# Optimization experiments

Measured on AMD Instinct MI355X. Metric: run time of the kernel, lower is better.

The kernel has to match this reference:

```python
import jax, jax.numpy as jnp
import numpy as np

N_HEADS = 8
EPSILON = -50000.0


def setup_inputs() -> dict:
    key = jax.random.key(0)
    k1, k2, k3, k4, k5, k6 = jax.random.split(key, 6)
    B, S, D = 4, 2048, 512
    q_vec = jax.random.normal(k1, (B, S, D), dtype=jnp.float32)
    k_mat = jax.random.normal(k2, (B, S, D), dtype=jnp.float32)
    v_mat = jax.random.normal(k3, (B, S, D), dtype=jnp.float32)
    # mask: mostly valid keys with some padding masked out
    mask = jax.random.uniform(k4, (B, S)) < 0.9
    cutoff = jax.random.uniform(k5, (B, S), dtype=jnp.float32)
    W_out = jax.random.normal(k6, (D, D), dtype=jnp.float32) * (1.0 / np.sqrt(D))
    return {"q_vec": q_vec, "k_mat": k_mat, "v_mat": v_mat,
            "mask": mask, "cutoff": cutoff, "W_out": W_out}


def reference(q_vec, k_mat, v_mat, mask, cutoff, W_out):
    D = q_vec.shape[-1]
    H = N_HEADS
    dh = D // H
    # split heads: [B, S, D] -> [B, S, H, dh]
    q_ = q_vec.reshape(q_vec.shape[:-1] + (H, dh))
    k_ = k_mat.reshape(k_mat.shape[:-1] + (H, dh))
    v_ = v_mat.reshape(v_mat.shape[:-1] + (H, dh))
    # scores: [B, H, Sq, Sk]
    scores = jnp.einsum('bqhd,bkhd->bhqk', q_, k_) / jnp.sqrt(jnp.asarray(dh, q_vec.dtype))
    # additive mask over keys, then stable softmax
    scores = jnp.where(mask[:, None, None, :], scores, EPSILON)
    probs = jax.nn.softmax(scores, axis=-1)
    # post-softmax cutoff scaling per key
    probs = probs * cutoff[:, None, None, :]
    # attention output: [B, Sq, H, dh] -> [B, Sq, D]
    att = jnp.einsum('bhqk,bkhd->bqhd', probs, v_).reshape(q_vec.shape)
    return att @ W_out
```

## Files before the change

kernel.cpp:

```cpp
#include <hip/hip_runtime.h>
#include <hip/hip_bf16.h>
#include <stdint.h>

#define B_ 4
#define S_ 2048
#define D_ 512
#define H_ 8

typedef __attribute__((ext_vector_type(4))) float f32x4;
typedef __attribute__((ext_vector_type(16))) float f32x16;
typedef __attribute__((ext_vector_type(8))) short s16x8;

__device__ __forceinline__ unsigned short f2bf(float x) {
  union { float f; unsigned u; } v; v.f = x;
  unsigned r = v.u + 0x7FFFu + ((v.u >> 16) & 1u);
  return (unsigned short)(r >> 16);
}

__device__ __forceinline__ unsigned cvtpk_bf16(float lo, float hi) {
  unsigned r;
  asm("v_cvt_pk_bf16_f32 %0, %1, %2" : "=v"(r) : "v"(lo), "v"(hi));
  return r;
}

__device__ __forceinline__ void plswap(unsigned &a, unsigned &b) {
  asm("v_permlane32_swap_b32 %0, %1" : "+v"(a), "+v"(b));
}

__device__ __forceinline__ void gload16(const void* g, void* lds) {
  __builtin_amdgcn_global_load_lds(
      (const __attribute__((address_space(1))) void*)g,
      (__attribute__((address_space(3))) void*)lds, 16, 0, 0);
}

__global__ __launch_bounds__(256) void conv_kv_kernel(
    const float* __restrict__ km, const float* __restrict__ vm,
    const float* __restrict__ cut, const int* __restrict__ mask,
    unsigned short* __restrict__ Kbf, unsigned short* __restrict__ Vt,
    unsigned short* __restrict__ fmg)
{
  const int st = blockIdx.x, bh = blockIdx.y;
  const int b = bh >> 3, h = bh & 7;
  const int s0 = st * 64;
  __shared__ unsigned short sT[64][68];
  const int tid = threadIdx.x;
#pragma unroll
  for (int j = 0; j < 4; ++j) {
    const int li = tid + j * 256;
    const int r  = li >> 4;
    const int c4 = (li & 15) * 4;
    const size_t g = ((size_t)(b * S_ + s0 + r)) * D_ + h * 64 + c4;
    const float4 kv = *(const float4*)(km + g);
    const float4 vv = *(const float4*)(vm + g);
    const int mk = mask[(size_t)b * S_ + s0 + r];
    const float f = mk ? cut[(size_t)b * S_ + s0 + r] : 0.f;
    *(ushort4*)(Kbf + ((size_t)(bh * S_ + s0 + r)) * 64 + c4) =
        make_ushort4(f2bf(kv.x), f2bf(kv.y), f2bf(kv.z), f2bf(kv.w));
    sT[r][c4 + 0] = f2bf(vv.x * f);
    sT[r][c4 + 1] = f2bf(vv.y * f);
    sT[r][c4 + 2] = f2bf(vv.z * f);
    sT[r][c4 + 3] = f2bf(vv.w * f);
    if (h == 0 && c4 == 0)
      fmg[(size_t)b * S_ + s0 + r] = mk ? (unsigned short)0x3F80 : (unsigned short)0;
  }
  __syncthreads();
#pragma unroll
  for (int j = 0; j < 4; ++j) {
    const int li = tid + j * 256;
    const int dh = li >> 4;
    const int s4 = (li & 15) * 4;
    *(ushort4*)(Vt + ((size_t)(bh * 64 + dh)) * S_ + s0 + s4) =
        make_ushort4(sT[s4 + 0][dh], sT[s4 + 1][dh], sT[s4 + 2][dh], sT[s4 + 3][dh]);
  }
}

__global__ __launch_bounds__(256) void conv_w_kernel(
    const float* __restrict__ W, unsigned short* __restrict__ Wt)
{
  const int k0 = blockIdx.x * 64, n0 = blockIdx.y * 64;
  __shared__ unsigned short sT[64][68];
  const int tid = threadIdx.x;
#pragma unroll
  for (int j = 0; j < 4; ++j) {
    const int li = tid + j * 256;
    const int r  = li >> 4;
    const int c4 = (li & 15) * 4;
    const float4 wv = *(const float4*)(W + (size_t)(k0 + r) * 512 + n0 + c4);
    sT[r][c4 + 0] = f2bf(wv.x);
    sT[r][c4 + 1] = f2bf(wv.y);
    sT[r][c4 + 2] = f2bf(wv.z);
    sT[r][c4 + 3] = f2bf(wv.w);
  }
  __syncthreads();
#pragma unroll
  for (int j = 0; j < 4; ++j) {
    const int li = tid + j * 256;
    const int n  = li >> 4;
    const int k4 = (li & 15) * 4;
    *(ushort4*)(Wt + (size_t)(n0 + n) * 512 + k0 + k4) =
        make_ushort4(sT[k4 + 0][n], sT[k4 + 1][n], sT[k4 + 2][n], sT[k4 + 3][n]);
  }
}

__global__ __launch_bounds__(256, 2) void attn_mfma_kernel(
    const float* __restrict__ qv, const unsigned short* __restrict__ Kbf,
    const unsigned short* __restrict__ Vt, const unsigned short* __restrict__ fmg,
    unsigned short* __restrict__ attb)
{
  __shared__ unsigned short sK[2][2][4096];
  __shared__ unsigned short sV[2][2][4096];

  const int qt = blockIdx.x, bh = blockIdx.y;
  const int b = bh >> 3, h = bh & 7;
  const int tid = threadIdx.x, w = tid >> 6, l = tid & 63;
  const int l31 = l & 31, hi = l >> 5;
  const int qh = w & 1, kh = w >> 1;
  const int kbase = kh * 1024;

  s16x8 qf[2][4];
#pragma unroll
  for (int s = 0; s < 2; ++s) {
    const int qrow = qt * 128 + qh * 64 + s * 32 + l31;
    const float* qp = qv + ((size_t)(b * S_ + qrow)) * D_ + h * 64 + hi * 8;
#pragma unroll
    for (int kc = 0; kc < 4; ++kc) {
      const float4 a0 = *(const float4*)(qp + kc * 16);
      const float4 a1 = *(const float4*)(qp + kc * 16 + 4);
      union { unsigned u[4]; s16x8 v; } t;
      t.u[0] = cvtpk_bf16(a0.x * 0.125f, a0.y * 0.125f);
      t.u[1] = cvtpk_bf16(a0.z * 0.125f, a0.w * 0.125f);
      t.u[2] = cvtpk_bf16(a1.x * 0.125f, a1.y * 0.125f);
      t.u[3] = cvtpk_bf16(a1.z * 0.125f, a1.w * 0.125f);
      qf[s][kc] = t.v;
    }
  }

  f32x16 o00, o01, o10, o11, la0, la1;
#pragma unroll
  for (int r = 0; r < 16; ++r) {
    o00[r] = 0.f; o01[r] = 0.f; o10[r] = 0.f; o11[r] = 0.f;
    la0[r] = 0.f; la1[r] = 0.f;
  }

  const int swl = ((l & 7) ^ (l >> 3)) * 16;
  const int r8  = l >> 3;
  const char* KbfB = (const char*)(Kbf + (size_t)bh * S_ * 64);
  const char* VtB  = (const char*)(Vt + (size_t)bh * 64 * S_);

  auto STAGE = [&](int bufi, int kt) {
    const int k0 = kbase + kt * 64;
#pragma unroll
    for (int c = 0; c < 4; ++c) {
      const int chunk = qh * 4 + c;
      const int row = chunk * 8 + r8;
      gload16(KbfB + (size_t)(k0 + row) * 128 + swl, (char*)sK[kh][bufi] + chunk * 1024);
      gload16(VtB + ((size_t)row * S_ + k0) * 2 + swl, (char*)sV[kh][bufi] + chunk * 1024);
    }
  };

  STAGE(0, 0);
  __syncthreads();

  int buf = 0;
  for (int kt = 0; kt < 16; ++kt) {
    const int k0 = kbase + kt * 64;
    s16x8 fmf[4];
#pragma unroll
    for (int ks = 0; ks < 4; ++ks)
      fmf[ks] = *(const s16x8*)(fmg + (size_t)b * S_ + k0 + ks * 16 + hi * 8);

    if (kt + 1 < 16) STAGE(buf ^ 1, kt + 1);

    const char* pK = (const char*)sK[kh][buf];
    const char* pV = (const char*)sV[kh][buf];

    s16x8 pa[2][4];
#pragma unroll
    for (int k2 = 0; k2 < 2; ++k2) {
      f32x16 sa0, sa1;
#pragma unroll
      for (int r = 0; r < 16; ++r) { sa0[r] = 0.f; sa1[r] = 0.f; }
      __builtin_amdgcn_s_setprio(1);
#pragma unroll
      for (int kc = 0; kc < 4; ++kc) {
        const int row = k2 * 32 + l31;
        const s16x8 kf = *(const s16x8*)(pK + row * 128 +
                          ((kc * 32 + hi * 16) ^ ((row & 7) << 4)));
        sa0 = __builtin_amdgcn_mfma_f32_32x32x16_bf16(kf, qf[0][kc], sa0, 0, 0, 0);
        sa1 = __builtin_amdgcn_mfma_f32_32x32x16_bf16(kf, qf[1][kc], sa1, 0, 0, 0);
      }
      __builtin_amdgcn_s_setprio(0);
      float p0[16], p1[16];
#pragma unroll
      for (int r = 0; r < 16; ++r) { p0[r] = __expf(sa0[r]); p1[r] = __expf(sa1[r]); }
#pragma unroll
      for (int ks = 0; ks < 2; ++ks) {
        const int rb = ks * 8;
        {
          unsigned a0 = cvtpk_bf16(p0[rb + 0], p0[rb + 1]);
          unsigned a1 = cvtpk_bf16(p0[rb + 2], p0[rb + 3]);
          unsigned b0 = cvtpk_bf16(p0[rb + 4], p0[rb + 5]);
          unsigned b1 = cvtpk_bf16(p0[rb + 6], p0[rb + 7]);
          plswap(a0, b0); plswap(a1, b1);
          union { unsigned u[4]; s16x8 v; } t;
          t.u[0] = a0; t.u[1] = a1; t.u[2] = b0; t.u[3] = b1;
          pa[0][k2 * 2 + ks] = t.v;
        }
        {
          unsigned a0 = cvtpk_bf16(p1[rb + 0], p1[rb + 1]);
          unsigned a1 = cvtpk_bf16(p1[rb + 2], p1[rb + 3]);
          unsigned b0 = cvtpk_bf16(p1[rb + 4], p1[rb + 5]);
          unsigned b1 = cvtpk_bf16(p1[rb + 6], p1[rb + 7]);
          plswap(a0, b0); plswap(a1, b1);
          union { unsigned u[4]; s16x8 v; } t;
          t.u[0] = a0; t.u[1] = a1; t.u[2] = b0; t.u[3] = b1;
          pa[1][k2 * 2 + ks] = t.v;
        }
      }
    }

    __builtin_amdgcn_s_setprio(1);
#pragma unroll
    for (int ks2 = 0; ks2 < 4; ++ks2) {
      const int cb = ks2 * 32 + hi * 16;
      const int rv0 = l31, rv1 = 32 + l31;
      const s16x8 vb0 = *(const s16x8*)(pV + rv0 * 128 + (cb ^ ((rv0 & 7) << 4)));
      const s16x8 vb1 = *(const s16x8*)(pV + rv1 * 128 + (cb ^ ((rv1 & 7) << 4)));
      o00 = __builtin_amdgcn_mfma_f32_32x32x16_bf16(pa[0][ks2], vb0, o00, 0, 0, 0);
      o01 = __builtin_amdgcn_mfma_f32_32x32x16_bf16(pa[0][ks2], vb1, o01, 0, 0, 0);
      o10 = __builtin_amdgcn_mfma_f32_32x32x16_bf16(pa[1][ks2], vb0, o10, 0, 0, 0);
      o11 = __builtin_amdgcn_mfma_f32_32x32x16_bf16(pa[1][ks2], vb1, o11, 0, 0, 0);
      la0 = __builtin_amdgcn_mfma_f32_32x32x16_bf16(pa[0][ks2], fmf[ks2], la0, 0, 0, 0);
      la1 = __builtin_amdgcn_mfma_f32_32x32x16_bf16(pa[1][ks2], fmf[ks2], la1, 0, 0, 0);
    }
    __builtin_amdgcn_s_setprio(0);

    __syncthreads();
    buf ^= 1;
  }

  float* po = (float*)&sK[0][0][0];
  float* pl = (float*)&sV[0][0][0];

  if (kh == 0) {
#pragma unroll
    for (int half = 0; half < 2; ++half)
#pragma unroll
      for (int r = 0; r < 16; ++r) {
        po[(((qh * 2 + 0) * 2 + half) * 16 + r) * 64 + l] = (half == 0) ? o00[r] : o01[r];
        po[(((qh * 2 + 1) * 2 + half) * 16 + r) * 64 + l] = (half == 0) ? o10[r] : o11[r];
      }
    if (l31 == 0) {
#pragma unroll
      for (int r = 0; r < 16; ++r) {
        pl[((qh * 2 + 0) * 2 + hi) * 16 + r] = la0[r];
        pl[((qh * 2 + 1) * 2 + hi) * 16 + r] = la1[r];
      }
    }
  }
  __syncthreads();
  if (kh == 1) {
#pragma unroll
    for (int half = 0; half < 2; ++half)
#pragma unroll
      for (int r = 0; r < 16; ++r) {
        po[(((qh * 2 + 0) * 2 + half) * 16 + r) * 64 + l] += (half == 0) ? o00[r] : o01[r];
        po[(((qh * 2 + 1) * 2 + half) * 16 + r) * 64 + l] += (half == 0) ? o10[r] : o11[r];
      }
    if (l31 == 0) {
#pragma unroll
      for (int r = 0; r < 16; ++r) {
        pl[((qh * 2 + 0) * 2 + hi) * 16 + r] += la0[r];
        pl[((qh * 2 + 1) * 2 + hi) * 16 + r] += la1[r];
      }
    }
  }
  __syncthreads();

  const int qm = w & 1, sm = w >> 1;
  unsigned short* ob = attb + ((size_t)b * S_) * D_ + h * 64;
#pragma unroll
  for (int r = 0; r < 16; ++r) {
    const float ls = pl[((qm * 2 + sm) * 2 + hi) * 16 + r];
    const float inv = 1.f / ls;
    const int q = qt * 128 + qm * 64 + sm * 32 + (r & 3) + 8 * (r >> 2) + 4 * hi;
#pragma unroll
    for (int half = 0; half < 2; ++half) {
      const float ov = po[(((qm * 2 + sm) * 2 + half) * 16 + r) * 64 + l];
      ob[(size_t)q * D_ + half * 32 + l31] = f2bf(ov * inv);
    }
  }
}

__global__ __launch_bounds__(256) void proj_mfma_kernel(
    const unsigned short* __restrict__ A, const unsigned short* __restrict__ Wt,
    float* __restrict__ out)
{
  __shared__ unsigned short sA[128 * 64];
  __shared__ unsigned short sB[128 * 64];
  const int m0 = blockIdx.x * 128, n0 = blockIdx.y * 128;
  const int tid = threadIdx.x, w = tid >> 6, l = tid & 63;
  const int l15 = l & 15, l4 = l >> 4;
  const int wm = (w >> 1) * 64, wn = (w & 1) * 64;
  const int swl = ((l & 7) ^ (l >> 3)) * 16;
  const int r8 = l >> 3;

  f32x4 acc[4][4];
#pragma unroll
  for (int i = 0; i < 4; ++i)
#pragma unroll
    for (int j = 0; j < 4; ++j) acc[i][j] = (f32x4){0.f, 0.f, 0.f, 0.f};

  for (int kt = 0; kt < 8; ++kt) {
    const int k0 = kt * 64;
    __syncthreads();
#pragma unroll
    for (int c = 0; c < 4; ++c) {
      const int chunk = w * 4 + c;
      const int r = chunk * 8 + r8;
      gload16((const char*)(A + ((size_t)(m0 + r)) * 512 + k0) + swl,
              (char*)sA + chunk * 1024);
      gload16((const char*)(Wt + ((size_t)(n0 + r)) * 512 + k0) + swl,
              (char*)sB + chunk * 1024);
    }
    __syncthreads();
#pragma unroll
    for (int ks = 0; ks < 2; ++ks) {
      s16x8 af[4], bf_[4];
#pragma unroll
      for (int mb = 0; mb < 4; ++mb) {
        const int row = wm + mb * 16 + l15;
        const int sz = (row & 7) << 4;
        af[mb] = *(const s16x8*)((const char*)sA + row * 128 + ((ks * 64 + l4 * 16) ^ sz));
      }
#pragma unroll
      for (int nb = 0; nb < 4; ++nb) {
        const int row = wn + nb * 16 + l15;
        const int sz = (row & 7) << 4;
        bf_[nb] = *(const s16x8*)((const char*)sB + row * 128 + ((ks * 64 + l4 * 16) ^ sz));
      }
#pragma unroll
      for (int mb = 0; mb < 4; ++mb)
#pragma unroll
        for (int nb = 0; nb < 4; ++nb)
          acc[mb][nb] = __builtin_amdgcn_mfma_f32_16x16x32_bf16(af[mb], bf_[nb], acc[mb][nb], 0, 0, 0);
    }
  }
#pragma unroll
  for (int mb = 0; mb < 4; ++mb)
#pragma unroll
    for (int nb = 0; nb < 4; ++nb)
#pragma unroll
      for (int r = 0; r < 4; ++r)
        out[(size_t)(m0 + wm + mb * 16 + l4 * 4 + r) * 512 + n0 + wn + nb * 16 + l15] =
            acc[mb][nb][r];
}

extern "C" void kernel_launch(void* const* d_in, const int* in_sizes, int n_in,
                              void* d_out, int out_size, void* d_ws, size_t ws_size,
                              hipStream_t stream) {
  const float* q    = (const float*)d_in[0];
  const float* k    = (const float*)d_in[1];
  const float* v    = (const float*)d_in[2];
  const int*   mask = (const int*)d_in[3];
  const float* cut  = (const float*)d_in[4];
  const float* W    = (const float*)d_in[5];
  float* out = (float*)d_out;

  char* ws = (char*)d_ws;
  unsigned short* Kbf  = (unsigned short*)(ws);
  unsigned short* Vt   = (unsigned short*)(ws + (8u << 20));
  unsigned short* attb = (unsigned short*)(ws + (16u << 20));
  unsigned short* Wt   = (unsigned short*)(ws + (24u << 20));
  unsigned short* fmg  = (unsigned short*)(ws + (25u << 20));

  conv_kv_kernel<<<dim3(S_ / 64, B_ * H_), 256, 0, stream>>>(k, v, cut, mask, Kbf, Vt, fmg);
  conv_w_kernel<<<dim3(8, 8), 256, 0, stream>>>(W, Wt);
  attn_mfma_kernel<<<dim3(S_ / 128, B_ * H_), 256, 0, stream>>>(q, Kbf, Vt, fmg, attb);
  proj_mfma_kernel<<<dim3(64, 4), 256, 0, stream>>>(attb, Wt, out);
}
```

Before: 79.62 us.

## Halve attention query tile, use exp2 and scalar row-sum instead of MFMA sum

After: 104.6 us. 1.31x slower.

```diff
diff --git a/kernel.cpp b/kernel.cpp
--- a/kernel.cpp
+++ b/kernel.cpp
@@ -27,6 +27,12 @@
   asm("v_permlane32_swap_b32 %0, %1" : "+v"(a), "+v"(b));
 }
 
+__device__ __forceinline__ float fexp2(float x) {
+  float r;
+  asm("v_exp_f32 %0, %1" : "=v"(r) : "v"(x));
+  return r;
+}
+
 __device__ __forceinline__ void gload16(const void* g, void* lds) {
   __builtin_amdgcn_global_load_lds(
       (const __attribute__((address_space(1))) void*)g,
@@ -37,7 +43,7 @@
     const float* __restrict__ km, const float* __restrict__ vm,
     const float* __restrict__ cut, const int* __restrict__ mask,
     unsigned short* __restrict__ Kbf, unsigned short* __restrict__ Vt,
-    unsigned short* __restrict__ fmg)
+    float* __restrict__ fmgf)
 {
   const int st = blockIdx.x, bh = blockIdx.y;
   const int b = bh >> 3, h = bh & 7;
@@ -61,7 +67,7 @@
     sT[r][c4 + 2] = f2bf(vv.z * f);
     sT[r][c4 + 3] = f2bf(vv.w * f);
     if (h == 0 && c4 == 0)
-      fmg[(size_t)b * S_ + s0 + r] = mk ? (unsigned short)0x3F80 : (unsigned short)0;
+      fmgf[(size_t)b * S_ + s0 + r] = mk ? 1.0f : 0.0f;
   }
   __syncthreads();
 #pragma unroll
@@ -102,12 +108,12 @@
   }
 }
 
-__global__ __launch_bounds__(256, 2) void attn_mfma_kernel(
+__global__ __launch_bounds__(256, 3) void attn_mfma_kernel(
     const float* __restrict__ qv, const unsigned short* __restrict__ Kbf,
-    const unsigned short* __restrict__ Vt, const unsigned short* __restrict__ fmg,
+    const unsigned short* __restrict__ Vt, const float* __restrict__ fmgf,
     unsigned short* __restrict__ attb)
 {
-  __shared__ unsigned short sK[2][2][4096];
+  __shared__ unsigned short sK[2][2][2048];
   __shared__ unsigned short sV[2][2][4096];
 
   const int qt = blockIdx.x, bh = blockIdx.y;
@@ -117,178 +123,161 @@
   const int qh = w & 1, kh = w >> 1;
   const int kbase = kh * 1024;
 
-  s16x8 qf[2][4];
-#pragma unroll
-  for (int s = 0; s < 2; ++s) {
-    const int qrow = qt * 128 + qh * 64 + s * 32 + l31;
+  s16x8 qf[4];
+  {
+    const float QS = 0.125f * 1.44269504088896f;
+    const int qrow = qt * 64 + qh * 32 + l31;
     const float* qp = qv + ((size_t)(b * S_ + qrow)) * D_ + h * 64 + hi * 8;
 #pragma unroll
     for (int kc = 0; kc < 4; ++kc) {
       const float4 a0 = *(const float4*)(qp + kc * 16);
       const float4 a1 = *(const float4*)(qp + kc * 16 + 4);
       union { unsigned u[4]; s16x8 v; } t;
-      t.u[0] = cvtpk_bf16(a0.x * 0.125f, a0.y * 0.125f);
-      t.u[1] = cvtpk_bf16(a0.z * 0.125f, a0.w * 0.125f);
-      t.u[2] = cvtpk_bf16(a1.x * 0.125f, a1.y * 0.125f);
-      t.u[3] = cvtpk_bf16(a1.z * 0.125f, a1.w * 0.125f);
-      qf[s][kc] = t.v;
-    }
-  }
-
-  f32x16 o00, o01, o10, o11, la0, la1;
-#pragma unroll
-  for (int r = 0; r < 16; ++r) {
-    o00[r] = 0.f; o01[r] = 0.f; o10[r] = 0.f; o11[r] = 0.f;
-    la0[r] = 0.f; la1[r] = 0.f;
-  }
+      t.u[0] = cvtpk_bf16(a0.x * QS, a0.y * QS);
+      t.u[1] = cvtpk_bf16(a0.z * QS, a0.w * QS);
+      t.u[2] = cvtpk_bf16(a1.x * QS, a1.y * QS);
+      t.u[3] = cvtpk_bf16(a1.z * QS, a1.w * QS);
+      qf[kc] = t.v;
+    }
+  }
+
+  f32x16 o0, o1;
+  float lsum = 0.f;
+#pragma unroll
+  for (int r = 0; r < 16; ++r) { o0[r] = 0.f; o1[r] = 0.f; }
 
   const int swl = ((l & 7) ^ (l >> 3)) * 16;
   const int r8  = l >> 3;
   const char* KbfB = (const char*)(Kbf + (size_t)bh * S_ * 64);
   const char* VtB  = (const char*)(Vt + (size_t)bh * 64 * S_);
-
-  auto STAGE = [&](int bufi, int kt) {
-    const int k0 = kbase + kt * 64;
+  const float* fmB = fmgf + (size_t)b * S_;
+
+  auto STAGE_K = [&](int kt, int bufi) {
+    const int k0 = kbase + kt * 32;
+#pragma unroll
+    for (int c = 0; c < 2; ++c) {
+      const int chunk = qh * 2 + c;
+      const int row = chunk * 8 + r8;
+      gload16(KbfB + (size_t)(k0 + row) * 128 + swl,
+              (char*)sK[kh][bufi] + chunk * 1024);
+    }
+  };
+  auto STAGE_V = [&](int vt, int bufi) {
+    const int k0 = kbase + vt * 64;
 #pragma unroll
     for (int c = 0; c < 4; ++c) {
       const int chunk = qh * 4 + c;
       const int row = chunk * 8 + r8;
-      gload16(KbfB + (size_t)(k0 + row) * 128 + swl, (char*)sK[kh][bufi] + chunk * 1024);
-      gload16(VtB + ((size_t)row * S_ + k0) * 2 + swl, (char*)sV[kh][bufi] + chunk * 1024);
+      gload16(VtB + ((size_t)row * S_ + k0) * 2 + swl,
+              (char*)sV[kh][bufi] + chunk * 1024);
     }
   };
 
-  STAGE(0, 0);
-  __syncthreads();
-
-  int buf = 0;
-  for (int kt = 0; kt < 16; ++kt) {
-    const int k0 = kbase + kt * 64;
-    s16x8 fmf[4];
-#pragma unroll
-    for (int ks = 0; ks < 4; ++ks)
-      fmf[ks] = *(const s16x8*)(fmg + (size_t)b * S_ + k0 + ks * 16 + hi * 8);
-
-    if (kt + 1 < 16) STAGE(buf ^ 1, kt + 1);
-
-    const char* pK = (const char*)sK[kh][buf];
-    const char* pV = (const char*)sV[kh][buf];
-
-    s16x8 pa[2][4];
-#pragma unroll
-    for (int k2 = 0; k2 < 2; ++k2) {
-      f32x16 sa0, sa1;
-#pragma unroll
-      for (int r = 0; r < 16; ++r) { sa0[r] = 0.f; sa1[r] = 0.f; }
-      __builtin_amdgcn_s_setprio(1);
-#pragma unroll
-      for (int kc = 0; kc < 4; ++kc) {
-        const int row = k2 * 32 + l31;
-        const s16x8 kf = *(const s16x8*)(pK + row * 128 +
-                          ((kc * 32 + hi * 16) ^ ((row & 7) << 4)));
-        sa0 = __builtin_amdgcn_mfma_f32_32x32x16_bf16(kf, qf[0][kc], sa0, 0, 0, 0);
-        sa1 = __builtin_amdgcn_mfma_f32_32x32x16_bf16(kf, qf[1][kc], sa1, 0, 0, 0);
-      }
-      __builtin_amdgcn_s_setprio(0);
-      float p0[16], p1[16];
-#pragma unroll
-      for (int r = 0; r < 16; ++r) { p0[r] = __expf(sa0[r]); p1[r] = __expf(sa1[r]); }
-#pragma unroll
-      for (int ks = 0; ks < 2; ++ks) {
-        const int rb = ks * 8;
-        {
-          unsigned a0 = cvtpk_bf16(p0[rb + 0], p0[rb + 1]);
-          unsigned a1 = cvtpk_bf16(p0[rb + 2], p0[rb + 3]);
-          unsigned b0 = cvtpk_bf16(p0[rb + 4], p0[rb + 5]);
-          unsigned b1 = cvtpk_bf16(p0[rb + 6], p0[rb + 7]);
-          plswap(a0, b0); plswap(a1, b1);
-          union { unsigned u[4]; s16x8 v; } t;
-          t.u[0] = a0; t.u[1] = a1; t.u[2] = b0; t.u[3] = b1;
-          pa[0][k2 * 2 + ks] = t.v;
-        }
-        {
-          unsigned a0 = cvtpk_bf16(p1[rb + 0], p1[rb + 1]);
-          unsigned a1 = cvtpk_bf16(p1[rb + 2], p1[rb + 3]);
-          unsigned b0 = cvtpk_bf16(p1[rb + 4], p1[rb + 5]);
-          unsigned b1 = cvtpk_bf16(p1[rb + 6], p1[rb + 7]);
-          plswap(a0, b0); plswap(a1, b1);
-          union { unsigned u[4]; s16x8 v; } t;
-          t.u[0] = a0; t.u[1] = a1; t.u[2] = b0; t.u[3] = b1;
-          pa[1][k2 * 2 + ks] = t.v;
-        }
-      }
-    }
-
+  STAGE_K(0, 0);
+  STAGE_V(0, 0);
+  __syncthreads();
+
+  int kb = 0, vbuf = 0;
+  for (int kt = 0; kt < 32; ++kt) {
+    const int half = kt & 1, vt = kt >> 1;
+    if (kt + 1 < 32) STAGE_K(kt + 1, kb ^ 1);
+    if (half == 1 && vt + 1 < 16) STAGE_V(vt + 1, vbuf ^ 1);
+
+    const char* pK = (const char*)sK[kh][kb];
+    const char* pV = (const char*)sV[kh][vbuf];
+
+    f32x16 sa;
+#pragma unroll
+    for (int r = 0; r < 16; ++r) sa[r] = 0.f;
     __builtin_amdgcn_s_setprio(1);
 #pragma unroll
-    for (int ks2 = 0; ks2 < 4; ++ks2) {
-      const int cb = ks2 * 32 + hi * 16;
+    for (int kc = 0; kc < 4; ++kc) {
+      const s16x8 kf = *(const s16x8*)(pK + l31 * 128 +
+                        ((kc * 32 + hi * 16) ^ ((l31 & 7) << 4)));
+      sa = __builtin_amdgcn_mfma_f32_32x32x16_bf16(kf, qf[kc], sa, 0, 0, 0);
+    }
+    __builtin_amdgcn_s_setprio(0);
+
+    const int kg0 = kbase + kt * 32;
+    float4 fm4[4];
+#pragma unroll
+    for (int j = 0; j < 4; ++j)
+      fm4[j] = *(const float4*)(fmB + kg0 + j * 8 + hi * 4);
+    float p[16];
+#pragma unroll
+    for (int r = 0; r < 16; ++r) p[r] = fexp2(sa[r]);
+#pragma unroll
+    for (int j = 0; j < 4; ++j) {
+      lsum = fmaf(p[j * 4 + 0], fm4[j].x, lsum);
+      lsum = fmaf(p[j * 4 + 1], fm4[j].y, lsum);
+      lsum = fmaf(p[j * 4 + 2], fm4[j].z, lsum);
+      lsum = fmaf(p[j * 4 + 3], fm4[j].w, lsum);
+    }
+
+    s16x8 pa[2];
+#pragma unroll
+    for (int ks = 0; ks < 2; ++ks) {
+      const int rb = ks * 8;
+      unsigned a0 = cvtpk_bf16(p[rb + 0], p[rb + 1]);
+      unsigned a1 = cvtpk_bf16(p[rb + 2], p[rb + 3]);
+      unsigned b0 = cvtpk_bf16(p[rb + 4], p[rb + 5]);
+      unsigned b1 = cvtpk_bf16(p[rb + 6], p[rb + 7]);
+      plswap(a0, b0); plswap(a1, b1);
+      union { unsigned u[4]; s16x8 v; } t;
+      t.u[0] = a0; t.u[1] = a1; t.u[2] = b0; t.u[3] = b1;
+      pa[ks] = t.v;
+    }
+
+    __builtin_amdgcn_s_setprio(1);
+#pragma unroll
+    for (int ks = 0; ks < 2; ++ks) {
+      const int cb = (half * 2 + ks) * 32 + hi * 16;
       const int rv0 = l31, rv1 = 32 + l31;
       const s16x8 vb0 = *(const s16x8*)(pV + rv0 * 128 + (cb ^ ((rv0 & 7) << 4)));
       const s16x8 vb1 = *(const s16x8*)(pV + rv1 * 128 + (cb ^ ((rv1 & 7) << 4)));
-      o00 = __builtin_amdgcn_mfma_f32_32x32x16_bf16(pa[0][ks2], vb0, o00, 0, 0, 0);
-      o01 = __builtin_amdgcn_mfma_f32_32x32x16_bf16(pa[0][ks2], vb1, o01, 0, 0, 0);
-      o10 = __builtin_amdgcn_mfma_f32_32x32x16_bf16(pa[1][ks2], vb0, o10, 0, 0, 0);
-      o11 = __builtin_amdgcn_mfma_f32_32x32x16_bf16(pa[1][ks2], vb1, o11, 0, 0, 0);
-      la0 = __builtin_amdgcn_mfma_f32_32x32x16_bf16(pa[0][ks2], fmf[ks2], la0, 0, 0, 0);
-      la1 = __builtin_amdgcn_mfma_f32_32x32x16_bf16(pa[1][ks2], fmf[ks2], la1, 0, 0, 0);
+      o0 = __builtin_amdgcn_mfma_f32_32x32x16_bf16(pa[ks], vb0, o0, 0, 0, 0);
+      o1 = __builtin_amdgcn_mfma_f32_32x32x16_bf16(pa[ks], vb1, o1, 0, 0, 0);
     }
     __builtin_amdgcn_s_setprio(0);
 
     __syncthreads();
-    buf ^= 1;
-  }
+    kb ^= 1;
+    vbuf ^= half;
+  }
+
+  const float lt = lsum + __shfl_xor(lsum, 32);
 
   float* po = (float*)&sK[0][0][0];
   float* pl = (float*)&sV[0][0][0];
 
   if (kh == 0) {
 #pragma unroll
-    for (int half = 0; half < 2; ++half)
-#pragma unroll
-      for (int r = 0; r < 16; ++r) {
-        po[(((qh * 2 + 0) * 2 + half) * 16 + r) * 64 + l] = (half == 0) ? o00[r] : o01[r];
-        po[(((qh * 2 + 1) * 2 + half) * 16 + r) * 64 + l] = (half == 0) ? o10[r] : o11[r];
-      }
-    if (l31 == 0) {
-#pragma unroll
-      for (int r = 0; r < 16; ++r) {
-        pl[((qh * 2 + 0) * 2 + hi) * 16 + r] = la0[r];
-        pl[((qh * 2 + 1) * 2 + hi) * 16 + r] = la1[r];
-      }
-    }
+    for (int r = 0; r < 16; ++r) {
+      po[((qh * 2 + 0) * 16 + r) * 64 + l] = o0[r];
+      po[((qh * 2 + 1) * 16 + r) * 64 + l] = o1[r];
+    }
+    if (hi == 0) pl[qh * 32 + l31] = lt;
   }
   __syncthreads();
   if (kh == 1) {
 #pragma unroll
-    for (int half = 0; half < 2; ++half)
-#pragma unroll
-      for (int r = 0; r < 16; ++r) {
-        po[(((qh * 2 + 0) * 2 + half) * 16 + r) * 64 + l] += (half == 0) ? o00[r] : o01[r];
-        po[(((qh * 2 + 1) * 2 + half) * 16 + r) * 64 + l] += (half == 0) ? o10[r] : o11[r];
-      }
-    if (l31 == 0) {
-#pragma unroll
-      for (int r = 0; r < 16; ++r) {
-        pl[((qh * 2 + 0) * 2 + hi) * 16 + r] += la0[r];
-        pl[((qh * 2 + 1) * 2 + hi) * 16 + r] += la1[r];
-      }
-    }
-  }
-  __syncthreads();
-
-  const int qm = w & 1, sm = w >> 1;
+    for (int r = 0; r < 16; ++r) {
+      po[((qh * 2 + 0) * 16 + r) * 64 + l] += o0[r];
+      po[((qh * 2 + 1) * 16 + r) * 64 + l] += o1[r];
+    }
+    if (hi == 0) pl[qh * 32 + l31] += lt;
+  }
+  __syncthreads();
+
+  const int qh_o = w & 1, sm = w >> 1;
   unsigned short* ob = attb + ((size_t)b * S_) * D_ + h * 64;
 #pragma unroll
   for (int r = 0; r < 16; ++r) {
-    const float ls = pl[((qm * 2 + sm) * 2 + hi) * 16 + r];
-    const float inv = 1.f / ls;
-    const int q = qt * 128 + qm * 64 + sm * 32 + (r & 3) + 8 * (r >> 2) + 4 * hi;
-#pragma unroll
-    for (int half = 0; half < 2; ++half) {
-      const float ov = po[(((qm * 2 + sm) * 2 + half) * 16 + r) * 64 + l];
-      ob[(size_t)q * D_ + half * 32 + l31] = f2bf(ov * inv);
-    }
+    const int qloc = (r & 3) + 8 * (r >> 2) + 4 * hi;
+    const float inv = 1.f / pl[qh_o * 32 + qloc];
+    const float ov = po[((qh_o * 2 + sm) * 16 + r) * 64 + l];
+    const int q = qt * 64 + qh_o * 32 + qloc;
+    ob[(size_t)q * D_ + sm * 32 + l31] = f2bf(ov * inv);
   }
 }
 
@@ -372,10 +361,10 @@
   unsigned short* Vt   = (unsigned short*)(ws + (8u << 20));
   unsigned short* attb = (unsigned short*)(ws + (16u << 20));
   unsigned short* Wt   = (unsigned short*)(ws + (24u << 20));
-  unsigned short* fmg  = (unsigned short*)(ws + (25u << 20));
-
-  conv_kv_kernel<<<dim3(S_ / 64, B_ * H_), 256, 0, stream>>>(k, v, cut, mask, Kbf, Vt, fmg);
+  float*          fmgf = (float*)(ws + (25u << 20));
+
+  conv_kv_kernel<<<dim3(S_ / 64, B_ * H_), 256, 0, stream>>>(k, v, cut, mask, Kbf, Vt, fmgf);
   conv_w_kernel<<<dim3(8, 8), 256, 0, stream>>>(W, Wt);
-  attn_mfma_kernel<<<dim3(S_ / 128, B_ * H_), 256, 0, stream>>>(q, Kbf, Vt, fmg, attb);
+  attn_mfma_kernel<<<dim3(S_ / 64, B_ * H_), 256, 0, stream>>>(q, Kbf, Vt, fmgf, attb);
   proj_mfma_kernel<<<dim3(64, 4), 256, 0, stream>>>(attb, Wt, out);
 }
```
